# Kernel tuning notes

Hardware: AMD Instinct MI355X
Metric: run time of the kernel (lower is better)

## Reference

```python
import jax, jax.numpy as jnp
import numpy as np

N, T, H = 4000, 32, 64      # N = batch_size*n_neurons, t_repetition, gcn_d
E = 1024000
NT = N * T                   # graph nodes after temporal unrolling
N_NEURONS = 500
B = N // N_NEURONS
T_EBD = 16                   # tau * t_repetition = 0.5*32
N_STEPS = 12


def setup_inputs() -> dict:
    key = jax.random.key(0)
    ks = jax.random.split(key, 13)
    s = 1.0 / np.sqrt(H)
    return {
        "node_features": jax.random.normal(ks[0], (N, T, H), jnp.float32),
        "edge_index_batch": jax.random.randint(ks[1], (2, E), 0, NT, jnp.int32),
        "edge_attr_batch": jax.random.uniform(ks[2], (E,), jnp.float32),
        "batch": jax.random.randint(ks[3], (N,), 0, B, jnp.int32),
        # GRU params (1 layer, torch layout: W_ih [3H,H], W_hh [3H,H])
        "gru_Wih": jax.random.normal(ks[4], (3 * H, H), jnp.float32) * s,
        "gru_Whh": jax.random.normal(ks[5], (3 * H, H), jnp.float32) * s,
        "gru_bih": jax.random.normal(ks[6], (3 * H,), jnp.float32) * s,
        "gru_bhh": jax.random.normal(ks[7], (3 * H,), jnp.float32) * s,
        # GCNConv linear weight [out,in], no bias
        "gcn_W": jax.random.normal(ks[8], (H, H), jnp.float32) * s,
        # temporal attention MLP: Linear(T->T_ebd), Linear(T_ebd->T), no bias
        "attn_W1": jax.random.normal(ks[9], (T_EBD, T), jnp.float32) * (1.0 / np.sqrt(T)),
        "attn_W2": jax.random.normal(ks[10], (T, T_EBD), jnp.float32) * (1.0 / np.sqrt(T_EBD)),
        # final head Linear(gcn_d -> n_steps) with bias
        "fc_W": jax.random.normal(ks[11], (N_STEPS, H), jnp.float32) * s,
        "fc_b": jax.random.normal(ks[12], (N_STEPS,), jnp.float32) * s,
    }


def _gru(x, Wih, Whh, bih, bhh):
    # x: [N, T, H] -> outputs [N, T, H] (torch GRU equations, h0 = 0)
    xg = x @ Wih.T + bih  # [N, T, 3H], input projection precomputed

    def step(h, xg_t):
        hg = h @ Whh.T + bhh
        xr, xz, xn = jnp.split(xg_t, 3, axis=-1)
        hr, hz, hn = jnp.split(hg, 3, axis=-1)
        r = jax.nn.sigmoid(xr + hr)
        z = jax.nn.sigmoid(xz + hz)
        n = jnp.tanh(xn + r * hn)
        h_new = (1.0 - z) * n + z * h
        return h_new, h_new

    h0 = jnp.zeros((x.shape[0], Whh.shape[1]), x.dtype)
    _, hs = jax.lax.scan(step, h0, jnp.swapaxes(xg, 0, 1))  # hs: [T, N, H]
    return jnp.swapaxes(hs, 0, 1)


def _gcn(x, W, edge_index, edge_weight, n_nodes):
    # PyG GCNConv: add self-loops (weight 1), symmetric deg^-1/2 norm, no bias
    loops = jnp.arange(n_nodes, dtype=edge_index.dtype)
    src = jnp.concatenate([edge_index[0], loops])
    dst = jnp.concatenate([edge_index[1], loops])
    w = jnp.concatenate([edge_weight, jnp.ones((n_nodes,), edge_weight.dtype)])
    xw = x @ W.T                                            # [NT, H]
    deg = jax.ops.segment_sum(w, dst, num_segments=n_nodes)
    dis = jnp.where(deg > 0, jax.lax.rsqrt(jnp.where(deg > 0, deg, 1.0)), 0.0)
    norm = dis[src] * w * dis[dst]                          # [E+NT]
    msgs = norm[:, None] * xw[src]                          # gather + scale
    return jax.ops.segment_sum(msgs, dst, num_segments=n_nodes)


def reference(node_features, edge_index_batch, edge_attr_batch, batch,
              gru_Wih, gru_Whh, gru_bih, gru_bhh, gcn_W,
              attn_W1, attn_W2, fc_W, fc_b):
    # DGRLayer: GRU over time, then GCN over the flattened (node,time) graph
    g = _gru(node_features, gru_Wih, gru_Whh, gru_bih, gru_bhh)  # [N, T, H]
    x = g.reshape(NT, H)
    x = _gcn(x, gcn_W, edge_index_batch, edge_attr_batch, NT)
    x3 = x.reshape(N, T, H)

    # TemporalAttention (reshape mirrors torch contiguous .view semantics)
    xt = x3.reshape(B, T, N_NEURONS * H).mean(axis=-1)           # [B, T]
    attn = jax.nn.sigmoid(jax.nn.relu(xt @ attn_W1.T) @ attn_W2.T)  # [B, T]

    nf = x3.reshape(B, T, N_NEURONS, H)
    pooled = jnp.sum(attn[:, :, None, None] * nf, axis=(1, 2))   # [B, H]
    return pooled @ fc_W.T + fc_b                                # [B, n_steps]
```

## Files before the change

### kernel.cpp

```cpp
#include <hip/hip_runtime.h>
#include <hip/hip_fp16.h>

#define NNODES   4000
#define TSTEPS   32
#define HDIM     64
#define ECOUNT   1024000
#define NTOT     128000
#define BATCHB   8
#define NNEUR    500
#define TEBD     16
#define NSTEPS   12

#define CNT_SHIFT 44
#define SUM_MASK  ((1ull << CNT_SHIFT) - 1ull)
#define SLOTS     32
#define REC_BLOCKS (NNODES / 16)

typedef _Float16 half8_t __attribute__((ext_vector_type(8)));
typedef float    f32x4_t __attribute__((ext_vector_type(4)));

__device__ __forceinline__ float sigmoidf_(float x) {
    return 1.0f / (1.0f + __expf(-x));
}
__device__ __forceinline__ float tanhf_(float x) {
    return 1.0f - 2.0f / (1.0f + __expf(2.0f * x));
}

__global__ __launch_bounds__(256) void k_recHist(
    const float* __restrict__ x, const float* __restrict__ Wih,
    const float* __restrict__ Whh, const float* __restrict__ bih,
    const float* __restrict__ bhh, const float* __restrict__ Wg,
    _Float16* __restrict__ xwh,
    const int* __restrict__ ei, const float* __restrict__ ea,
    unsigned long long* __restrict__ dc, int2* __restrict__ se32)
{
    __shared__ __align__(16) _Float16 hbuf[2][16 * 72];

    const int tid = threadIdx.x;

    if (blockIdx.x >= REC_BLOCKS) {
        int e = (blockIdx.x - REC_BLOCKS) * 256 + tid;
        int s = ei[e], d = ei[ECOUNT + e];
        float w = ea[e];
        unsigned long long fx = (unsigned long long)(w * 4294967296.0f + 0.5f);
        unsigned long long old = atomicAdd(&dc[d], (1ull << CNT_SHIFT) | fx);
        int r = (int)(old >> CNT_SHIFT);
        if (r < SLOTS)
            se32[d * SLOTS + r] = make_int2(s, __float_as_int(w));
        return;
    }

    const int lane = tid & 63;
    const int wv   = tid >> 6;
    const int c    = lane & 15;
    const int quad = lane >> 4;
    const int n0   = blockIdx.x * 16;

    auto makeB = [&](const float* W, int row, int k0) -> half8_t {
        const float4* p = (const float4*)(W + (size_t)row * HDIM + k0);
        float4 u = p[0], v = p[1];
        half8_t h;
        h[0] = (_Float16)u.x; h[1] = (_Float16)u.y; h[2] = (_Float16)u.z; h[3] = (_Float16)u.w;
        h[4] = (_Float16)v.x; h[5] = (_Float16)v.y; h[6] = (_Float16)v.z; h[7] = (_Float16)v.w;
        return h;
    };

    half8_t Bxr[2], Bxz[2], Bxn[2], Bhr[2], Bhz[2], Bhn[2], Bw[2];
#pragma unroll
    for (int kt = 0; kt < 2; ++kt) {
        int k0 = kt * 32 + quad * 8;
        Bxr[kt] = makeB(Wih, wv * 16 + c, k0);
        Bxz[kt] = makeB(Wih, 64 + wv * 16 + c, k0);
        Bxn[kt] = makeB(Wih, 128 + wv * 16 + c, k0);
        Bhr[kt] = makeB(Whh, wv * 16 + c, k0);
        Bhz[kt] = makeB(Whh, 64 + wv * 16 + c, k0);
        Bhn[kt] = makeB(Whh, 128 + wv * 16 + c, k0);
        Bw[kt]  = makeB(Wg, wv * 16 + c, k0);
    }

    const int f = wv * 16 + c;
    const float brz_r = bih[f] + bhh[f];
    const float brz_z = bih[64 + f] + bhh[64 + f];
    const float bin_  = bih[128 + f];
    const float bhn_  = bhh[128 + f];

    float hreg[4] = {0.f, 0.f, 0.f, 0.f};
    half8_t ah[2];

    const float* xp = x + (size_t)(n0 + c) * (TSTEPS * HDIM) + quad * 8;

    float4 xq0[4], xq1[4];
    {
        const float* p0 = xp;
        xq0[0] = *(const float4*)(p0);      xq0[1] = *(const float4*)(p0 + 4);
        xq0[2] = *(const float4*)(p0 + 32); xq0[3] = *(const float4*)(p0 + 36);
        const float* p1 = xp + HDIM;
        xq1[0] = *(const float4*)(p1);      xq1[1] = *(const float4*)(p1 + 4);
        xq1[2] = *(const float4*)(p1 + 32); xq1[3] = *(const float4*)(p1 + 36);
    }

    auto step = [&](int t, float4* xq) {
        half8_t ax[2];
#pragma unroll
        for (int kt = 0; kt < 2; ++kt) {
            float4 u = xq[kt * 2], v = xq[kt * 2 + 1];
            half8_t a;
            a[0] = (_Float16)u.x; a[1] = (_Float16)u.y; a[2] = (_Float16)u.z; a[3] = (_Float16)u.w;
            a[4] = (_Float16)v.x; a[5] = (_Float16)v.y; a[6] = (_Float16)v.z; a[7] = (_Float16)v.w;
            ax[kt] = a;
        }
        if (t + 2 < TSTEPS) {
            const float* pt = xp + (size_t)(t + 2) * HDIM;
            xq[0] = *(const float4*)(pt);      xq[1] = *(const float4*)(pt + 4);
            xq[2] = *(const float4*)(pt + 32); xq[3] = *(const float4*)(pt + 36);
        }

        f32x4_t Cr  = (f32x4_t){0.f, 0.f, 0.f, 0.f};
        f32x4_t Cz  = (f32x4_t){0.f, 0.f, 0.f, 0.f};
        f32x4_t Cnx = (f32x4_t){0.f, 0.f, 0.f, 0.f};
        f32x4_t Cnh = (f32x4_t){0.f, 0.f, 0.f, 0.f};

#pragma unroll
        for (int kt = 0; kt < 2; ++kt) {
            Cr  = __builtin_amdgcn_mfma_f32_16x16x32_f16(ax[kt], Bxr[kt], Cr, 0, 0, 0);
            Cz  = __builtin_amdgcn_mfma_f32_16x16x32_f16(ax[kt], Bxz[kt], Cz, 0, 0, 0);
            Cnx = __builtin_amdgcn_mfma_f32_16x16x32_f16(ax[kt], Bxn[kt], Cnx, 0, 0, 0);
        }
        if (t > 0) {
#pragma unroll
            for (int kt = 0; kt < 2; ++kt) {
                Cr  = __builtin_amdgcn_mfma_f32_16x16x32_f16(ah[kt], Bhr[kt], Cr, 0, 0, 0);
                Cz  = __builtin_amdgcn_mfma_f32_16x16x32_f16(ah[kt], Bhz[kt], Cz, 0, 0, 0);
                Cnh = __builtin_amdgcn_mfma_f32_16x16x32_f16(ah[kt], Bhn[kt], Cnh, 0, 0, 0);
            }
        }

        _Float16* hb = hbuf[t & 1];
#pragma unroll
        for (int r = 0; r < 4; ++r) {
            float rr = sigmoidf_(Cr[r] + brz_r);
            float zz = sigmoidf_(Cz[r] + brz_z);
            float nn = tanhf_(Cnx[r] + bin_ + rr * (Cnh[r] + bhn_));
            float hn = (1.0f - zz) * nn + zz * hreg[r];
            hreg[r] = hn;
            hb[(quad * 4 + r) * 72 + f] = (_Float16)hn;
        }

        __syncthreads();

#pragma unroll
        for (int kt = 0; kt < 2; ++kt)
            ah[kt] = *(half8_t*)&hb[c * 72 + kt * 32 + quad * 8];

        f32x4_t Cw = (f32x4_t){0.f, 0.f, 0.f, 0.f};
#pragma unroll
        for (int kt = 0; kt < 2; ++kt)
            Cw = __builtin_amdgcn_mfma_f32_16x16x32_f16(ah[kt], Bw[kt], Cw, 0, 0, 0);

#pragma unroll
        for (int r = 0; r < 4; ++r) {
            int row = (n0 + quad * 4 + r) * TSTEPS + t;
            xwh[(size_t)row * HDIM + f] = (_Float16)Cw[r];
        }
    };

#pragma unroll 1
    for (int tt = 0; tt < TSTEPS; tt += 2) {
        step(tt, xq0);
        step(tt + 1, xq1);
    }
}

__global__ __launch_bounds__(256) void k_gather(
    const _Float16* __restrict__ xwh, const unsigned long long* __restrict__ dc,
    const int2* __restrict__ se32, float* __restrict__ S)
{
    const int tid  = threadIdx.x;
    const int lane = tid & 63;
    const int d = blockIdx.x * 4 + (tid >> 6);

    const unsigned long long pk = dc[d];
    const float dd = rsqrtf(1.0f + (float)(pk & SUM_MASK) * 0x1p-32f);
    int cnt = (int)(pk >> CNT_SHIFT);
    cnt = cnt < SLOTS ? cnt : SLOTS;
    const int2* bkt = se32 + (size_t)d * SLOTS;

    float a0 = dd * (float)xwh[(size_t)d * HDIM + lane];
    float a1 = 0.f, a2 = 0.f, a3 = 0.f;
    int j = 0;
    for (; j + 4 <= cnt; j += 4) {
        int2 e0 = bkt[j], e1 = bkt[j + 1], e2 = bkt[j + 2], e3 = bkt[j + 3];
        unsigned long long p0 = dc[e0.x], p1 = dc[e1.x];
        unsigned long long p2 = dc[e2.x], p3 = dc[e3.x];
        float c0 = rsqrtf(1.0f + (float)(p0 & SUM_MASK) * 0x1p-32f) * __int_as_float(e0.y);
        float c1 = rsqrtf(1.0f + (float)(p1 & SUM_MASK) * 0x1p-32f) * __int_as_float(e1.y);
        float c2 = rsqrtf(1.0f + (float)(p2 & SUM_MASK) * 0x1p-32f) * __int_as_float(e2.y);
        float c3 = rsqrtf(1.0f + (float)(p3 & SUM_MASK) * 0x1p-32f) * __int_as_float(e3.y);
        float v0 = (float)xwh[(size_t)e0.x * HDIM + lane];
        float v1 = (float)xwh[(size_t)e1.x * HDIM + lane];
        float v2 = (float)xwh[(size_t)e2.x * HDIM + lane];
        float v3 = (float)xwh[(size_t)e3.x * HDIM + lane];
        a0 = fmaf(c0, v0, a0);
        a1 = fmaf(c1, v1, a1);
        a2 = fmaf(c2, v2, a2);
        a3 = fmaf(c3, v3, a3);
    }
    for (; j < cnt; ++j) {
        int2 e = bkt[j];
        unsigned long long pe = dc[e.x];
        a0 = fmaf(rsqrtf(1.0f + (float)(pe & SUM_MASK) * 0x1p-32f) * __int_as_float(e.y),
                  (float)xwh[(size_t)e.x * HDIM + lane], a0);
    }

    __shared__ float red[256];
    red[tid] = dd * ((a0 + a1) + (a2 + a3));
    __syncthreads();
    if (tid < 64) {
        float s = red[tid] + red[64 + tid] + red[128 + tid] + red[192 + tid];
        atomicAdd(&S[((blockIdx.x * 4) / NNEUR) * HDIM + tid], s);
    }
}

__global__ __launch_bounds__(256) void k_final(
    const float* __restrict__ S, const float* __restrict__ W1,
    const float* __restrict__ W2, const float* __restrict__ fcW,
    const float* __restrict__ fcb, float* __restrict__ out)
{
    __shared__ float xt[256];
    __shared__ float a1[128];
    __shared__ float attn[256];
    __shared__ float pooled[512];
    const int tid = threadIdx.x;

    {
        float s = 0.f;
        const float* p = S + tid * 64;
#pragma unroll
        for (int hh = 0; hh < 64; ++hh) s += p[hh];
        xt[tid] = s * (1.0f / 32000.0f);
    }
    __syncthreads();
    if (tid < 128) {
        int b = tid >> 4, i = tid & 15;
        float s = 0.f;
#pragma unroll
        for (int t = 0; t < 32; ++t) s += xt[b * 32 + t] * W1[i * 32 + t];
        a1[tid] = fmaxf(s, 0.f);
    }
    __syncthreads();
    {
        int b = tid >> 5, t = tid & 31;
        float s = 0.f;
#pragma unroll
        for (int i = 0; i < 16; ++i) s += a1[b * 16 + i] * W2[t * 16 + i];
        attn[tid] = 1.0f / (1.0f + __expf(-s));
    }
    __syncthreads();
    for (int o = tid; o < 512; o += 256) {
        int b = o >> 6, h = o & 63;
        float s = 0.f;
#pragma unroll
        for (int t = 0; t < 32; ++t) s += attn[b * 32 + t] * S[(b * 32 + t) * 64 + h];
        pooled[o] = s;
    }
    __syncthreads();
    if (tid < BATCHB * NSTEPS) {
        int b = tid / NSTEPS, st = tid % NSTEPS;
        float acc = fcb[st];
#pragma unroll
        for (int h = 0; h < 64; ++h) acc += pooled[b * 64 + h] * fcW[st * 64 + h];
        out[b * NSTEPS + st] = acc;
    }
}

extern "C" void kernel_launch(void* const* d_in, const int* in_sizes, int n_in,
                              void* d_out, int out_size, void* d_ws, size_t ws_size,
                              hipStream_t stream) {
    const float* x   = (const float*)d_in[0];
    const int*   ei  = (const int*)  d_in[1];
    const float* ea  = (const float*)d_in[2];
    const float* Wih = (const float*)d_in[4];
    const float* Whh = (const float*)d_in[5];
    const float* bih = (const float*)d_in[6];
    const float* bhh = (const float*)d_in[7];
    const float* Wg  = (const float*)d_in[8];
    const float* W1  = (const float*)d_in[9];
    const float* W2  = (const float*)d_in[10];
    const float* fcW = (const float*)d_in[11];
    const float* fcb = (const float*)d_in[12];
    float* out = (float*)d_out;

    char* p = (char*)d_ws;
    unsigned long long* dc = (unsigned long long*)p; p += sizeof(unsigned long long) * NTOT;
    float* S = (float*)p;          p += sizeof(float) * 256 * HDIM;
    int2*  se32 = (int2*)p;        p += sizeof(int2) * (size_t)NTOT * SLOTS;
    _Float16* xwh = (_Float16*)p;  p += sizeof(_Float16) * (size_t)NTOT * HDIM;

    hipMemsetAsync(dc, 0, sizeof(unsigned long long) * NTOT + sizeof(float) * 256 * HDIM, stream);
    k_recHist <<<REC_BLOCKS + ECOUNT / 256, 256, 0, stream>>>(
        x, Wih, Whh, bih, bhh, Wg, xwh, ei, ea, dc, se32);
    k_gather  <<<NTOT / 4, 256, 0, stream>>>(xwh, dc, se32, S);
    k_final   <<<1, 256, 0, stream>>>(S, W1, W2, fcW, fcb, out);
}
```

Before: 271.3 us.

## Pack degree counters into 32-bit words and gather multiple rows per wave

The per-node degree/count accumulator shrinks from a 64-bit word (44-bit fixed-point sum) to a 32-bit word (23-bit sum at scale 2^18, count in the upper bits). This halves atomic and gather traffic on the counter array and lets it use 32-bit atomics. The gather kernel now processes five destination rows per wave and accumulates them locally before the block reduction, which cuts the block count and the number of global atomics into S. The cost is lower fixed-point precision on the degree sums and less parallelism per row.

New measurement: 236.5 us. -12.8%, faster.

```diff
diff --git a/kernel.cpp b/kernel.cpp
--- a/kernel.cpp
+++ b/kernel.cpp
@@ -11,10 +11,14 @@
 #define TEBD     16
 #define NSTEPS   12
 
-#define CNT_SHIFT 44
-#define SUM_MASK  ((1ull << CNT_SHIFT) - 1ull)
+#define CNT_SHIFT 23
+#define SUM_MASK  0x7FFFFFu
+#define SUM_SCALE 262144.0f
 #define SLOTS     32
 #define REC_BLOCKS (NNODES / 16)
+
+#define ROWS_PER_WAVE  5
+#define ROWS_PER_BLOCK 20
 
 typedef _Float16 half8_t __attribute__((ext_vector_type(8)));
 typedef float    f32x4_t __attribute__((ext_vector_type(4)));
@@ -32,7 +36,7 @@
     const float* __restrict__ bhh, const float* __restrict__ Wg,
     _Float16* __restrict__ xwh,
     const int* __restrict__ ei, const float* __restrict__ ea,
-    unsigned long long* __restrict__ dc, int2* __restrict__ se32)
+    unsigned* __restrict__ dc, int2* __restrict__ se32)
 {
     __shared__ __align__(16) _Float16 hbuf[2][16 * 72];
 
@@ -42,8 +46,8 @@
         int e = (blockIdx.x - REC_BLOCKS) * 256 + tid;
         int s = ei[e], d = ei[ECOUNT + e];
         float w = ea[e];
-        unsigned long long fx = (unsigned long long)(w * 4294967296.0f + 0.5f);
-        unsigned long long old = atomicAdd(&dc[d], (1ull << CNT_SHIFT) | fx);
+        unsigned fx = (unsigned)(w * SUM_SCALE + 0.5f);
+        unsigned old = atomicAdd(&dc[d], (1u << CNT_SHIFT) | fx);
         int r = (int)(old >> CNT_SHIFT);
         if (r < SLOTS)
             se32[d * SLOTS + r] = make_int2(s, __float_as_int(w));
@@ -172,52 +176,66 @@
 }
 
 __global__ __launch_bounds__(256) void k_gather(
-    const _Float16* __restrict__ xwh, const unsigned long long* __restrict__ dc,
+    const _Float16* __restrict__ xwh, const unsigned* __restrict__ dc,
     const int2* __restrict__ se32, float* __restrict__ S)
 {
     const int tid  = threadIdx.x;
     const int lane = tid & 63;
-    const int d = blockIdx.x * 4 + (tid >> 6);
-
-    const unsigned long long pk = dc[d];
-    const float dd = rsqrtf(1.0f + (float)(pk & SUM_MASK) * 0x1p-32f);
-    int cnt = (int)(pk >> CNT_SHIFT);
-    cnt = cnt < SLOTS ? cnt : SLOTS;
-    const int2* bkt = se32 + (size_t)d * SLOTS;
-
-    float a0 = dd * (float)xwh[(size_t)d * HDIM + lane];
-    float a1 = 0.f, a2 = 0.f, a3 = 0.f;
-    int j = 0;
-    for (; j + 4 <= cnt; j += 4) {
-        int2 e0 = bkt[j], e1 = bkt[j + 1], e2 = bkt[j + 2], e3 = bkt[j + 3];
-        unsigned long long p0 = dc[e0.x], p1 = dc[e1.x];
-        unsigned long long p2 = dc[e2.x], p3 = dc[e3.x];
-        float c0 = rsqrtf(1.0f + (float)(p0 & SUM_MASK) * 0x1p-32f) * __int_as_float(e0.y);
-        float c1 = rsqrtf(1.0f + (float)(p1 & SUM_MASK) * 0x1p-32f) * __int_as_float(e1.y);
-        float c2 = rsqrtf(1.0f + (float)(p2 & SUM_MASK) * 0x1p-32f) * __int_as_float(e2.y);
-        float c3 = rsqrtf(1.0f + (float)(p3 & SUM_MASK) * 0x1p-32f) * __int_as_float(e3.y);
-        float v0 = (float)xwh[(size_t)e0.x * HDIM + lane];
-        float v1 = (float)xwh[(size_t)e1.x * HDIM + lane];
-        float v2 = (float)xwh[(size_t)e2.x * HDIM + lane];
-        float v3 = (float)xwh[(size_t)e3.x * HDIM + lane];
-        a0 = fmaf(c0, v0, a0);
-        a1 = fmaf(c1, v1, a1);
-        a2 = fmaf(c2, v2, a2);
-        a3 = fmaf(c3, v3, a3);
-    }
-    for (; j < cnt; ++j) {
-        int2 e = bkt[j];
-        unsigned long long pe = dc[e.x];
-        a0 = fmaf(rsqrtf(1.0f + (float)(pe & SUM_MASK) * 0x1p-32f) * __int_as_float(e.y),
-                  (float)xwh[(size_t)e.x * HDIM + lane], a0);
+    const int wv   = tid >> 6;
+    const int d0   = blockIdx.x * ROWS_PER_BLOCK + wv * ROWS_PER_WAVE;
+
+    unsigned pk[ROWS_PER_WAVE];
+    float    sf[ROWS_PER_WAVE];
+#pragma unroll
+    for (int i = 0; i < ROWS_PER_WAVE; ++i) pk[i] = dc[d0 + i];
+#pragma unroll
+    for (int i = 0; i < ROWS_PER_WAVE; ++i)
+        sf[i] = (float)xwh[(size_t)(d0 + i) * HDIM + lane];
+
+    float acc = 0.f;
+#pragma unroll
+    for (int i = 0; i < ROWS_PER_WAVE; ++i) {
+        const int d = d0 + i;
+        const float dd = rsqrtf(1.0f + (float)(pk[i] & SUM_MASK) * 0x1p-18f);
+        int cnt = (int)(pk[i] >> CNT_SHIFT);
+        cnt = cnt < SLOTS ? cnt : SLOTS;
+        const int2* bkt = se32 + (size_t)d * SLOTS;
+
+        float a0 = dd * sf[i];
+        float a1 = 0.f, a2 = 0.f, a3 = 0.f;
+        int j = 0;
+        for (; j + 4 <= cnt; j += 4) {
+            int2 e0 = bkt[j], e1 = bkt[j + 1], e2 = bkt[j + 2], e3 = bkt[j + 3];
+            unsigned p0 = dc[e0.x], p1 = dc[e1.x];
+            unsigned p2 = dc[e2.x], p3 = dc[e3.x];
+            float c0 = rsqrtf(1.0f + (float)(p0 & SUM_MASK) * 0x1p-18f) * __int_as_float(e0.y);
+            float c1 = rsqrtf(1.0f + (float)(p1 & SUM_MASK) * 0x1p-18f) * __int_as_float(e1.y);
+            float c2 = rsqrtf(1.0f + (float)(p2 & SUM_MASK) * 0x1p-18f) * __int_as_float(e2.y);
+            float c3 = rsqrtf(1.0f + (float)(p3 & SUM_MASK) * 0x1p-18f) * __int_as_float(e3.y);
+            float v0 = (float)xwh[(size_t)e0.x * HDIM + lane];
+            float v1 = (float)xwh[(size_t)e1.x * HDIM + lane];
+            float v2 = (float)xwh[(size_t)e2.x * HDIM + lane];
+            float v3 = (float)xwh[(size_t)e3.x * HDIM + lane];
+            a0 = fmaf(c0, v0, a0);
+            a1 = fmaf(c1, v1, a1);
+            a2 = fmaf(c2, v2, a2);
+            a3 = fmaf(c3, v3, a3);
+        }
+        for (; j < cnt; ++j) {
+            int2 e = bkt[j];
+            unsigned pe = dc[e.x];
+            a0 = fmaf(rsqrtf(1.0f + (float)(pe & SUM_MASK) * 0x1p-18f) * __int_as_float(e.y),
+                      (float)xwh[(size_t)e.x * HDIM + lane], a0);
+        }
+        acc = fmaf(dd, (a0 + a1) + (a2 + a3), acc);
     }
 
     __shared__ float red[256];
-    red[tid] = dd * ((a0 + a1) + (a2 + a3));
+    red[tid] = acc;
     __syncthreads();
     if (tid < 64) {
         float s = red[tid] + red[64 + tid] + red[128 + tid] + red[192 + tid];
-        atomicAdd(&S[((blockIdx.x * 4) / NNEUR) * HDIM + tid], s);
+        atomicAdd(&S[((blockIdx.x * ROWS_PER_BLOCK) / NNEUR) * HDIM + tid], s);
     }
 }
 
@@ -291,14 +309,14 @@
     float* out = (float*)d_out;
 
     char* p = (char*)d_ws;
-    unsigned long long* dc = (unsigned long long*)p; p += sizeof(unsigned long long) * NTOT;
+    unsigned* dc = (unsigned*)p;   p += sizeof(unsigned) * NTOT;
     float* S = (float*)p;          p += sizeof(float) * 256 * HDIM;
     int2*  se32 = (int2*)p;        p += sizeof(int2) * (size_t)NTOT * SLOTS;
     _Float16* xwh = (_Float16*)p;  p += sizeof(_Float16) * (size_t)NTOT * HDIM;
 
-    hipMemsetAsync(dc, 0, sizeof(unsigned long long) * NTOT + sizeof(float) * 256 * HDIM, stream);
+    hipMemsetAsync(dc, 0, sizeof(unsigned) * NTOT + sizeof(float) * 256 * HDIM, stream);
     k_recHist <<<REC_BLOCKS + ECOUNT / 256, 256, 0, stream>>>(
         x, Wih, Whh, bih, bhh, Wg, xwh, ei, ea, dc, se32);
-    k_gather  <<<NTOT / 4, 256, 0, stream>>>(xwh, dc, se32, S);
+    k_gather  <<<NTOT / ROWS_PER_BLOCK, 256, 0, stream>>>(xwh, dc, se32, S);
     k_final   <<<1, 256, 0, stream>>>(S, W1, W2, fcW, fcb, out);
 }
```

## Replace per-destination bucketed gather with edge-parallel scatter into per-(batch,time) LDS accumulators

Applied to the files above, without the earlier changes.

The histogram pass now only accumulates a float weighted degree per destination node and no longer builds a capped 32-slot bucket list. Because the output only needs sums over neuron groups per (batch,time), a new edge kernel streams the edges directly and scatters the normalized source features into a shared-memory accumulator indexed by destination/500. Each block handles one half of the feature dimension and writes its partial sums to a workspace, and a merge kernel reduces those partials deterministically. This removes the bucket fill and the per-node gather with its random accesses to the degree array. In exchange it relies on LDS atomics and adds a large partial-sum buffer plus an extra kernel launch.

New measurement: 578.7 us. 113% more time.

```diff
diff --git a/kernel.cpp b/kernel.cpp
--- a/kernel.cpp
+++ b/kernel.cpp
@@ -11,10 +11,14 @@
 #define TEBD     16
 #define NSTEPS   12
 
-#define CNT_SHIFT 44
-#define SUM_MASK  ((1ull << CNT_SHIFT) - 1ull)
-#define SLOTS     32
-#define REC_BLOCKS (NNODES / 16)
+#define REC_BLOCKS  (NNODES / 16)
+#define HIST_BLOCKS (ECOUNT / 256)
+
+#define EPB   2048
+#define EDGE_BLOCKS_PER_HALF 500
+#define EDGE_BLOCKS (2 * EDGE_BLOCKS_PER_HALF)
+#define SELF_ROWS_PER_BLOCK 256
+#define PPART_STRIDE 8192
 
 typedef _Float16 half8_t __attribute__((ext_vector_type(8)));
 typedef float    f32x4_t __attribute__((ext_vector_type(4)));
@@ -32,7 +36,7 @@
     const float* __restrict__ bhh, const float* __restrict__ Wg,
     _Float16* __restrict__ xwh,
     const int* __restrict__ ei, const float* __restrict__ ea,
-    unsigned long long* __restrict__ dc, int2* __restrict__ se32)
+    float* __restrict__ dw)
 {
     __shared__ __align__(16) _Float16 hbuf[2][16 * 72];
 
@@ -40,13 +44,7 @@
 
     if (blockIdx.x >= REC_BLOCKS) {
         int e = (blockIdx.x - REC_BLOCKS) * 256 + tid;
-        int s = ei[e], d = ei[ECOUNT + e];
-        float w = ea[e];
-        unsigned long long fx = (unsigned long long)(w * 4294967296.0f + 0.5f);
-        unsigned long long old = atomicAdd(&dc[d], (1ull << CNT_SHIFT) | fx);
-        int r = (int)(old >> CNT_SHIFT);
-        if (r < SLOTS)
-            se32[d * SLOTS + r] = make_int2(s, __float_as_int(w));
+        atomicAdd(&dw[ei[ECOUNT + e]], ea[e]);
         return;
     }
 
@@ -171,54 +169,90 @@
     }
 }
 
-__global__ __launch_bounds__(256) void k_gather(
-    const _Float16* __restrict__ xwh, const unsigned long long* __restrict__ dc,
-    const int2* __restrict__ se32, float* __restrict__ S)
+__global__ __launch_bounds__(256) void k_edges(
+    const _Float16* __restrict__ xwh, const float* __restrict__ dw,
+    const int* __restrict__ ei, const float* __restrict__ ea,
+    float* __restrict__ Ppart)
 {
+    __shared__ float acc[256 * 32];
     const int tid  = threadIdx.x;
     const int lane = tid & 63;
-    const int d = blockIdx.x * 4 + (tid >> 6);
-
-    const unsigned long long pk = dc[d];
-    const float dd = rsqrtf(1.0f + (float)(pk & SUM_MASK) * 0x1p-32f);
-    int cnt = (int)(pk >> CNT_SHIFT);
-    cnt = cnt < SLOTS ? cnt : SLOTS;
-    const int2* bkt = se32 + (size_t)d * SLOTS;
-
-    float a0 = dd * (float)xwh[(size_t)d * HDIM + lane];
-    float a1 = 0.f, a2 = 0.f, a3 = 0.f;
-    int j = 0;
-    for (; j + 4 <= cnt; j += 4) {
-        int2 e0 = bkt[j], e1 = bkt[j + 1], e2 = bkt[j + 2], e3 = bkt[j + 3];
-        unsigned long long p0 = dc[e0.x], p1 = dc[e1.x];
-        unsigned long long p2 = dc[e2.x], p3 = dc[e3.x];
-        float c0 = rsqrtf(1.0f + (float)(p0 & SUM_MASK) * 0x1p-32f) * __int_as_float(e0.y);
-        float c1 = rsqrtf(1.0f + (float)(p1 & SUM_MASK) * 0x1p-32f) * __int_as_float(e1.y);
-        float c2 = rsqrtf(1.0f + (float)(p2 & SUM_MASK) * 0x1p-32f) * __int_as_float(e2.y);
-        float c3 = rsqrtf(1.0f + (float)(p3 & SUM_MASK) * 0x1p-32f) * __int_as_float(e3.y);
-        float v0 = (float)xwh[(size_t)e0.x * HDIM + lane];
-        float v1 = (float)xwh[(size_t)e1.x * HDIM + lane];
-        float v2 = (float)xwh[(size_t)e2.x * HDIM + lane];
-        float v3 = (float)xwh[(size_t)e3.x * HDIM + lane];
-        a0 = fmaf(c0, v0, a0);
-        a1 = fmaf(c1, v1, a1);
-        a2 = fmaf(c2, v2, a2);
-        a3 = fmaf(c3, v3, a3);
-    }
-    for (; j < cnt; ++j) {
-        int2 e = bkt[j];
-        unsigned long long pe = dc[e.x];
-        a0 = fmaf(rsqrtf(1.0f + (float)(pe & SUM_MASK) * 0x1p-32f) * __int_as_float(e.y),
-                  (float)xwh[(size_t)e.x * HDIM + lane], a0);
-    }
+    const int wv   = tid >> 6;
+    const int half = blockIdx.x & 1;
+    const int pb   = blockIdx.x >> 1;
+    const int h0   = half * 32;
+    const int hh   = lane & 31;
+    const int hi   = lane >> 5;
+
+    for (int i = tid; i < 256 * 32; i += 256) acc[i] = 0.f;
+    __syncthreads();
+
+    {
+        const int rbase = pb * SELF_ROWS_PER_BLOCK + wv * 64;
+        float dl = dw[rbase + lane];
+        float cs = 1.0f / (1.0f + dl);
+#pragma unroll
+        for (int i = 0; i < 32; ++i) {
+            float cA = __int_as_float(__builtin_amdgcn_readlane(__float_as_int(cs), 2 * i));
+            float cB = __int_as_float(__builtin_amdgcn_readlane(__float_as_int(cs), 2 * i + 1));
+            int row   = rbase + 2 * i + hi;
+            float myC = hi ? cB : cA;
+            float v = (float)xwh[(size_t)row * HDIM + h0 + hh];
+            atomicAdd(&acc[((unsigned)row / 500u) * 32 + hh], myC * v);
+        }
+    }
+
+    const int ebase = pb * EPB + wv * 64;
+#pragma unroll 1
+    for (int g = 0; g < EPB / 256; ++g) {
+        int e  = ebase + g * 256;
+        int s  = ei[e + lane];
+        int dv = ei[ECOUNT + e + lane];
+        float w = ea[e + lane];
+        float c = rsqrtf(1.0f + dw[s]) * w * rsqrtf(1.0f + dw[dv]);
+        int bt = (int)((unsigned)dv / 500u);
+#pragma unroll
+        for (int j = 0; j < 32; ++j) {
+            int   sA = __builtin_amdgcn_readlane(s, 2 * j);
+            int   sB = __builtin_amdgcn_readlane(s, 2 * j + 1);
+            float cA = __int_as_float(__builtin_amdgcn_readlane(__float_as_int(c), 2 * j));
+            float cB = __int_as_float(__builtin_amdgcn_readlane(__float_as_int(c), 2 * j + 1));
+            int   bA = __builtin_amdgcn_readlane(bt, 2 * j);
+            int   bB = __builtin_amdgcn_readlane(bt, 2 * j + 1);
+            int   mySrc = hi ? sB : sA;
+            float myC   = hi ? cB : cA;
+            int   myBt  = hi ? bB : bA;
+            float v = (float)xwh[(size_t)mySrc * HDIM + h0 + hh];
+            atomicAdd(&acc[myBt * 32 + hh], myC * v);
+        }
+    }
+
+    __syncthreads();
+    float* dst = Ppart + (size_t)blockIdx.x * PPART_STRIDE;
+    for (int i = tid; i < PPART_STRIDE; i += 256) dst[i] = acc[i];
+}
+
+__global__ __launch_bounds__(256) void k_merge(const float* __restrict__ Ppart,
+                                               float* __restrict__ S)
+{
+    const int bt  = blockIdx.x;
+    const int tid = threadIdx.x;
+    const int h   = tid & 63;
+    const int q   = tid >> 6;
+    const int half = h >> 5;
+    const int hh   = h & 31;
+
+    const float* base = Ppart + (size_t)half * PPART_STRIDE + bt * 32 + hh;
+    float s = 0.f;
+#pragma unroll 4
+    for (int pb = q * 125; pb < q * 125 + 125; ++pb)
+        s += base[(size_t)pb * 2 * PPART_STRIDE];
 
     __shared__ float red[256];
-    red[tid] = dd * ((a0 + a1) + (a2 + a3));
-    __syncthreads();
-    if (tid < 64) {
-        float s = red[tid] + red[64 + tid] + red[128 + tid] + red[192 + tid];
-        atomicAdd(&S[((blockIdx.x * 4) / NNEUR) * HDIM + tid], s);
-    }
+    red[tid] = s;
+    __syncthreads();
+    if (tid < 64)
+        S[bt * 64 + tid] = red[tid] + red[64 + tid] + red[128 + tid] + red[192 + tid];
 }
 
 __global__ __launch_bounds__(256) void k_final(
@@ -291,14 +325,15 @@
     float* out = (float*)d_out;
 
     char* p = (char*)d_ws;
-    unsigned long long* dc = (unsigned long long*)p; p += sizeof(unsigned long long) * NTOT;
-    float* S = (float*)p;          p += sizeof(float) * 256 * HDIM;
-    int2*  se32 = (int2*)p;        p += sizeof(int2) * (size_t)NTOT * SLOTS;
+    float* dw = (float*)p;         p += sizeof(float) * NTOT;
+    float* S  = (float*)p;         p += sizeof(float) * 256 * HDIM;
+    float* Ppart = (float*)p;      p += sizeof(float) * (size_t)EDGE_BLOCKS * PPART_STRIDE;
     _Float16* xwh = (_Float16*)p;  p += sizeof(_Float16) * (size_t)NTOT * HDIM;
 
-    hipMemsetAsync(dc, 0, sizeof(unsigned long long) * NTOT + sizeof(float) * 256 * HDIM, stream);
-    k_recHist <<<REC_BLOCKS + ECOUNT / 256, 256, 0, stream>>>(
-        x, Wih, Whh, bih, bhh, Wg, xwh, ei, ea, dc, se32);
-    k_gather  <<<NTOT / 4, 256, 0, stream>>>(xwh, dc, se32, S);
+    hipMemsetAsync(dw, 0, sizeof(float) * NTOT, stream);
+    k_recHist <<<REC_BLOCKS + HIST_BLOCKS, 256, 0, stream>>>(
+        x, Wih, Whh, bih, bhh, Wg, xwh, ei, ea, dw);
+    k_edges   <<<EDGE_BLOCKS, 256, 0, stream>>>(xwh, dw, ei, ea, Ppart);
+    k_merge   <<<256, 256, 0, stream>>>(Ppart, S);
     k_final   <<<1, 256, 0, stream>>>(S, W1, W2, fcW, fcb, out);
 }
```
